# Optimization experiments

Measured on AMD Instinct MI355X. Metric: run time of the kernel, lower is better.

## Reference

```python
import jax, jax.numpy as jnp
import numpy as np

B, S, D, H = 4, 1024, 1024, 16
DK = D // H


def _linear_params(key, scale):
    kw, kb = jax.random.split(key)
    W = jax.random.normal(kw, (D, D), dtype=jnp.float32) * scale
    b = jax.random.normal(kb, (D,), dtype=jnp.float32) * 0.01
    return W, b


def setup_inputs() -> dict:
    key = jax.random.key(0)
    ks = jax.random.split(key, 12)
    scale = 1.0 / np.sqrt(D)
    inp = {
        "query": jax.random.normal(ks[0], (B, S, D), dtype=jnp.float32),
        "key": jax.random.normal(ks[1], (B, S, D), dtype=jnp.float32),
        "value": jax.random.normal(ks[2], (B, S, D), dtype=jnp.float32),
        "time_k": jax.random.normal(ks[3], (B, S, D), dtype=jnp.float32),
        "time_v": jax.random.normal(ks[4], (B, S, D), dtype=jnp.float32),
        "mask": jnp.zeros((B, 1, S, S), dtype=jnp.float32),
    }
    names = ["Wq", "bq", "Wk", "bk", "Wv", "bv", "Wtk", "btk", "Wtv", "btv", "Wm", "bm"]
    for i in range(6):
        W, b = _linear_params(ks[5 + i], scale)
        inp[names[2 * i]] = W
        inp[names[2 * i + 1]] = b
    return inp


def _split_heads(x):
    # [B,S,D] -> [B,H,S,DK]
    b, s, _ = x.shape
    return x.reshape(b, s, H, DK).transpose(0, 2, 1, 3)


def reference(query, key, value, time_k, time_v, mask,
              Wq, bq, Wk, bk, Wv, bv, Wtk, btk, Wtv, btv, Wm, bm):
    q = _split_heads(query @ Wq + bq)
    k = _split_heads(key @ Wk + bk)
    v = _split_heads(value @ Wv + bv)
    t_k = _split_heads(time_k @ Wtk + btk)
    t_v = _split_heads(time_v @ Wtv + btv)

    # scores[b,h,i,j] = q_i . k_j + t_k_i . q_j  (note second term uses q on the key axis)
    scores = jnp.einsum("bhid,bhjd->bhij", q, k) + jnp.einsum("bhid,bhjd->bhij", t_k, q)
    # module divides by sqrt(d_model) (query.size(-1)), not sqrt(d_k)
    scores = scores / jnp.sqrt(jnp.float32(D)) + mask
    probs = jax.nn.softmax(scores, axis=-1)

    # dropout is identity (p=0 / eval); squeeze(-2) is a no-op for S>1
    context = jnp.einsum("bhij,bhjd->bhid", probs, v) + jnp.einsum("bhij,bhjd->bhid", probs, t_v)
    x = context.transpose(0, 2, 1, 3).reshape(query.shape[0], -1, D)
    return x @ Wm + bm
```

## Files before the change

kernel.cpp:

```cpp
#include <hip/hip_runtime.h>
#include <hip/hip_bf16.h>
#include <cstdint>
#include <cstddef>

typedef __bf16 bf16;
typedef bf16 bf16x8 __attribute__((ext_vector_type(8)));
typedef bf16 bf16x4 __attribute__((ext_vector_type(4)));
typedef float f32x4 __attribute__((ext_vector_type(4)));
typedef unsigned int u32;

#define DEV static __device__ __forceinline__

DEV f32x4 mfma16(bf16x8 a, bf16x8 b, f32x4 c) {
    return __builtin_amdgcn_mfma_f32_16x16x32_bf16(a, b, c, 0, 0, 0);
}

DEV f32x4 shflx4(f32x4 v, int m) {
    f32x4 r;
    for (int i = 0; i < 4; ++i) r[i] = __shfl_xor(v[i], m, 64);
    return r;
}

DEV bf16x8 cvt8(const float* p) {
    float4 f0 = *(const float4*)p;
    float4 f1 = *(const float4*)(p + 4);
    bf16x8 v;
    v[0] = (bf16)f0.x; v[1] = (bf16)f0.y; v[2] = (bf16)f0.z; v[3] = (bf16)f0.w;
    v[4] = (bf16)f1.x; v[5] = (bf16)f1.y; v[6] = (bf16)f1.z; v[7] = (bf16)f1.w;
    return v;
}

DEV void glo(const bf16* g, bf16* l) {
    __builtin_amdgcn_global_load_lds(
        (const __attribute__((address_space(1))) u32*)g,
        (__attribute__((address_space(3))) u32*)l,
        16, 0, 0);
}

struct PrepArgs {
    const float* w[10];
    const float* act[5];
    bf16* wt;
    bf16* maskt;
    bf16* actbf[5];
};

__global__ __launch_bounds__(256) void prep_kernel(PrepArgs p)
{
    const int z = blockIdx.z;
    const int t = threadIdx.x;
    if (z < 10) {
        __shared__ bf16 tile[64][72];
        const float* src = p.w[z];
        bf16* out = (z < 6) ? (p.wt + (size_t)z * 1024 * 1024)
                            : (p.maskt + (size_t)(z - 6) * 1024 * 1024);
        const int r = t >> 3, c8 = (t & 7) * 8;
        const int row0 = blockIdx.y * 64, col0 = blockIdx.x * 64;
        *(bf16x8*)&tile[r][c8]      = cvt8(&src[(size_t)(row0 + r) * 1024 + col0 + c8]);
        *(bf16x8*)&tile[r + 32][c8] = cvt8(&src[(size_t)(row0 + r + 32) * 1024 + col0 + c8]);
        __syncthreads();
        for (int half = 0; half < 2; ++half) {
            int rr = r + half * 32;
            bf16x8 v;
            for (int j = 0; j < 8; ++j) v[j] = tile[c8 + j][rr];
            *(bf16x8*)&out[(size_t)(col0 + rr) * 1024 + row0 + c8] = v;
        }
    } else {
        const float* src = p.act[z - 10];
        bf16* dst = p.actbf[z - 10];
        const size_t chunk = (size_t)(blockIdx.y * 16 + blockIdx.x) * 16384;
        for (int c = 0; c < 8; ++c) {
            const size_t off = chunk + (size_t)c * 2048 + (size_t)t * 8;
            *(bf16x8*)&dst[off] = cvt8(&src[off]);
        }
    }
}

__global__ __launch_bounds__(256) void vsum_kernel(bf16* __restrict__ a,
                                                   const bf16* __restrict__ b)
{
    const size_t off = ((size_t)blockIdx.x * 256 + threadIdx.x) * 16;
    for (int c = 0; c < 2; ++c) {
        bf16x8 x = *(const bf16x8*)&a[off + c * 8];
        bf16x8 y = *(const bf16x8*)&b[off + c * 8];
        bf16x8 s;
        for (int e = 0; e < 8; ++e) s[e] = (bf16)((float)x[e] + (float)y[e]);
        *(bf16x8*)&a[off + c * 8] = s;
    }
}

struct ProjArgs {
    const void* A[5];
    const void* A2[5];
    const bf16* W[5];
    const bf16* W2[5];
    const float* bias[5];
    const float* bias2[5];
    bf16* out[5];
    int vst[5];
};

template<bool AF32>
__global__ __launch_bounds__(256) void proj_gemm(ProjArgs pa)
{
    const int z = blockIdx.z;
    const void* A   = pa.A[z];
    const void* A2p = pa.A2[z];
    const bf16* W   = pa.W[z];
    const bf16* W2  = pa.W2[z];
    const int m0 = blockIdx.y * 128, n0 = blockIdx.x * 128;
    __shared__ bf16 As[128 * 64];
    __shared__ bf16 Bs[128 * 64];
    const int t = threadIdx.x, lane = t & 63, w = t >> 6;
    const int ln = lane & 15, qd = lane >> 4;
    const int wm0 = (w >> 1) * 64, wn0 = (w & 1) * 64;
    const int srow = t >> 1, shalf = (t & 1) * 32;
    const int sub0 = w * 4;
    const int r8 = lane >> 3, c8 = (lane & 7) * 8;
    f32x4 acc[4][4];
    for (int i = 0; i < 4; ++i)
        for (int j = 0; j < 4; ++j)
            acc[i][j] = (f32x4){0.f, 0.f, 0.f, 0.f};
    const int npair = A2p ? 2 : 1;
    for (int pair = 0; pair < npair; ++pair) {
        const void* Ap = pair ? A2p : A;
        const bf16* Wp = pair ? W2 : W;
        for (int ks = 0; ks < 16; ++ks) {
            const int bk = ks * 64;
            __syncthreads();
            for (int i = 0; i < 4; ++i) {
                const int row = (sub0 + i) * 8 + r8;
                glo(&Wp[(size_t)(n0 + row) * 1024 + bk + c8], &Bs[(sub0 + i) * 512]);
            }
            if (AF32) {
                const float* src = &((const float*)Ap)[(size_t)(m0 + srow) * 1024 + bk + shalf];
                bf16* dst = &As[srow * 64 + shalf];
                *(bf16x8*)(dst)      = cvt8(src);
                *(bf16x8*)(dst + 8)  = cvt8(src + 8);
                *(bf16x8*)(dst + 16) = cvt8(src + 16);
                *(bf16x8*)(dst + 24) = cvt8(src + 24);
            } else {
                const bf16* Ab = (const bf16*)Ap;
                for (int i = 0; i < 4; ++i) {
                    const int row = (sub0 + i) * 8 + r8;
                    glo(&Ab[(size_t)(m0 + row) * 1024 + bk + c8], &As[(sub0 + i) * 512]);
                }
            }
            __syncthreads();
            for (int kc = 0; kc < 2; ++kc) {
                bf16x8 af[4], bfr[4];
                for (int mi = 0; mi < 4; ++mi)
                    af[mi] = *(const bf16x8*)&As[(wm0 + mi * 16 + ln) * 64 + kc * 32 + qd * 8];
                for (int ni = 0; ni < 4; ++ni)
                    bfr[ni] = *(const bf16x8*)&Bs[(wn0 + ni * 16 + ln) * 64 + kc * 32 + qd * 8];
                for (int mi = 0; mi < 4; ++mi)
                    for (int ni = 0; ni < 4; ++ni)
                        acc[mi][ni] = mfma16(af[mi], bfr[ni], acc[mi][ni]);
            }
        }
    }
    const float* bias  = pa.bias[z];
    const float* bias2 = pa.bias2[z];
    bf16* out = pa.out[z];
    const int vst = pa.vst[z];
    for (int ni = 0; ni < 4; ++ni) {
        const int n = n0 + wn0 + ni * 16 + ln;
        const float bv = bias[n] + (bias2 ? bias2[n] : 0.0f);
        for (int mi = 0; mi < 4; ++mi) {
            const int mbase = m0 + wm0 + mi * 16 + qd * 4;
            f32x4 v = acc[mi][ni];
            if (vst) {
                const int b = mbase >> 10, s = mbase & 1023;
                bf16x4 pk;
                for (int r = 0; r < 4; ++r) pk[r] = (bf16)(v[r] + bv);
                *(bf16x4*)&out[((size_t)(b * 1024 + n)) * 1024 + s] = pk;
            } else {
                for (int r = 0; r < 4; ++r)
                    out[(size_t)(mbase + r) * 1024 + n] = (bf16)(v[r] + bv);
            }
        }
    }
}

__global__ __launch_bounds__(256, 4) void attn5_kernel(
    const bf16* __restrict__ Qb, const bf16* __restrict__ Kb, const bf16* __restrict__ TKb,
    const bf16* __restrict__ VsT, const bf16* __restrict__ maskT,
    bf16* __restrict__ ctx)
{
    const int h = blockIdx.x, it = blockIdx.y, b = blockIdx.z;
    const int i0 = it * 64;
    __shared__ bf16 Ks[64 * 64];
    __shared__ bf16 QJs[64 * 64];
    __shared__ bf16 Vs[64 * 64];
    __shared__ bf16 Ps[64][68];
    const int t = threadIdx.x, lane = t & 63, w = t >> 6;
    const int ln = lane & 15, qd = lane >> 4;
    const size_t baseQ = ((size_t)b * 1024) * 1024 + (size_t)h * 64;
    const size_t MMc = (size_t)1024 * 1024;

    bf16x8 qf[2], tkf[2];
    {
        const size_t row = (size_t)(i0 + w * 16 + ln);
        for (int kc = 0; kc < 2; ++kc) {
            qf[kc]  = *(const bf16x8*)&Qb [baseQ + row * 1024 + kc * 32 + qd * 8];
            tkf[kc] = *(const bf16x8*)&TKb[baseQ + row * 1024 + kc * 32 + qd * 8];
        }
    }

    f32x4 O[4];
    f32x4 psum = (f32x4){0.f, 0.f, 0.f, 0.f};
    for (int dc = 0; dc < 4; ++dc) O[dc] = (f32x4){0.f, 0.f, 0.f, 0.f};

    const float c1 = 0.045084439f;
    const float c2 = 1.442695041f;

    for (int jt = 0; jt < 16; ++jt) {
        const int j0 = jt * 64;
        __syncthreads();
        {
            const int rr = lane >> 3, cb = (lane & 7) * 8;
            for (int i = 0; i < 6; ++i) {
                const int u = w * 6 + i;
                if (u < 8) {
                    glo(&Kb[baseQ + (size_t)(j0 + u * 8 + rr) * 1024 + cb], &Ks[u * 512]);
                } else if (u < 16) {
                    const int s = u - 8;
                    glo(&Qb[baseQ + (size_t)(j0 + s * 8 + rr) * 1024 + cb], &QJs[s * 512]);
                } else {
                    const int s = u - 16;
                    glo(&VsT[((size_t)b * 1024 + h * 64 + s * 8 + rr) * 1024 + j0 + cb],
                        &Vs[s * 512]);
                }
            }
        }
        bf16x4 mv[4];
        {
            const int ibase = i0 + w * 16 + qd * 4;
            for (int jc = 0; jc < 4; ++jc)
                mv[jc] = *(const bf16x4*)&maskT[(size_t)b * MMc +
                          (size_t)(j0 + jc * 16 + ln) * 1024 + ibase];
        }
        __syncthreads();

        f32x4 sc[4];
        for (int jc = 0; jc < 4; ++jc) {
            bf16x8 kf[2], qjf[2];
            for (int kc = 0; kc < 2; ++kc) {
                kf[kc]  = *(const bf16x8*)&Ks [(jc * 16 + ln) * 64 + kc * 32 + qd * 8];
                qjf[kc] = *(const bf16x8*)&QJs[(jc * 16 + ln) * 64 + kc * 32 + qd * 8];
            }
            f32x4 a = (f32x4){0.f, 0.f, 0.f, 0.f};
            a = mfma16(qf[0], kf[0], a);
            a = mfma16(qf[1], kf[1], a);
            a = mfma16(tkf[0], qjf[0], a);
            a = mfma16(tkf[1], qjf[1], a);
            sc[jc] = a;
        }
        const int ibl = w * 16 + qd * 4;
        for (int jc = 0; jc < 4; ++jc) {
            const int jl = jc * 16 + ln;
            for (int r = 0; r < 4; ++r) {
                const float p = exp2f(fmaf(sc[jc][r], c1, (float)mv[jc][r] * c2));
                psum[r] += p;
                Ps[ibl + r][jl] = (bf16)p;
            }
        }
        for (int kc = 0; kc < 2; ++kc) {
            bf16x4 lo = *(const bf16x4*)&Ps[w * 16 + ln][kc * 32 + qd * 8];
            bf16x4 hi = *(const bf16x4*)&Ps[w * 16 + ln][kc * 32 + qd * 8 + 4];
            bf16x8 pa;
            for (int e = 0; e < 4; ++e) { pa[e] = lo[e]; pa[4 + e] = hi[e]; }
            for (int dc = 0; dc < 4; ++dc) {
                bf16x8 vf = *(const bf16x8*)&Vs[(dc * 16 + ln) * 64 + kc * 32 + qd * 8];
                O[dc] = mfma16(pa, vf, O[dc]);
            }
        }
    }

    for (int m = 1; m <= 8; m <<= 1) psum += shflx4(psum, m);
    f32x4 rl;
    for (int r = 0; r < 4; ++r) rl[r] = 1.0f / psum[r];
    const int ibase = i0 + w * 16 + qd * 4;
    for (int dc = 0; dc < 4; ++dc) {
        const int d = h * 64 + dc * 16 + ln;
        f32x4 v = O[dc] * rl;
        for (int r = 0; r < 4; ++r)
            ctx[((size_t)b * 1024 + ibase + r) * 1024 + d] = (bf16)v[r];
    }
}

__global__ __launch_bounds__(256) void out_gemm(
    const bf16* __restrict__ A, const bf16* __restrict__ W,
    const float* __restrict__ bias, float* __restrict__ out)
{
    const int n0 = blockIdx.x * 128, m0 = blockIdx.y * 64;
    __shared__ bf16 As[64 * 64];
    __shared__ bf16 Bs[128 * 64];
    const int t = threadIdx.x, lane = t & 63, w = t >> 6;
    const int ln = lane & 15, qd = lane >> 4;
    const int wn0 = w * 32;
    const int rr = lane >> 3, cb = (lane & 7) * 8;
    f32x4 acc[4][2];
    for (int i = 0; i < 4; ++i)
        for (int j = 0; j < 2; ++j)
            acc[i][j] = (f32x4){0.f, 0.f, 0.f, 0.f};
    for (int ks = 0; ks < 16; ++ks) {
        const int bk = ks * 64;
        __syncthreads();
        for (int i = 0; i < 6; ++i) {
            const int u = w * 6 + i;
            if (u < 8) {
                const int r8 = u * 8 + rr;
                glo(&A[(size_t)(m0 + r8) * 1024 + bk + cb], &As[u * 512]);
            } else {
                const int sub = u - 8, r8 = sub * 8 + rr;
                glo(&W[(size_t)(n0 + r8) * 1024 + bk + cb], &Bs[sub * 512]);
            }
        }
        __syncthreads();
        for (int kc = 0; kc < 2; ++kc) {
            bf16x8 af[4], bfr[2];
            for (int mi = 0; mi < 4; ++mi)
                af[mi] = *(const bf16x8*)&As[(mi * 16 + ln) * 64 + kc * 32 + qd * 8];
            for (int ni = 0; ni < 2; ++ni)
                bfr[ni] = *(const bf16x8*)&Bs[(wn0 + ni * 16 + ln) * 64 + kc * 32 + qd * 8];
            for (int mi = 0; mi < 4; ++mi)
                for (int ni = 0; ni < 2; ++ni)
                    acc[mi][ni] = mfma16(af[mi], bfr[ni], acc[mi][ni]);
        }
    }
    for (int ni = 0; ni < 2; ++ni) {
        const int n = n0 + wn0 + ni * 16 + ln;
        const float bv = bias[n];
        for (int mi = 0; mi < 4; ++mi) {
            const int mbase = m0 + mi * 16 + qd * 4;
            f32x4 v = acc[mi][ni];
            for (int r = 0; r < 4; ++r)
                out[(size_t)(mbase + r) * 1024 + n] = v[r] + bv;
        }
    }
}

extern "C" void kernel_launch(void* const* d_in, const int* in_sizes, int n_in,
                              void* d_out, int out_size, void* d_ws, size_t ws_size,
                              hipStream_t stream)
{
    (void)in_sizes; (void)n_in; (void)out_size;
    const float* query  = (const float*)d_in[0];
    const float* key    = (const float*)d_in[1];
    const float* value  = (const float*)d_in[2];
    const float* time_k = (const float*)d_in[3];
    const float* time_v = (const float*)d_in[4];
    const float* mask   = (const float*)d_in[5];
    const float* Wq  = (const float*)d_in[6];  const float* bq  = (const float*)d_in[7];
    const float* Wk  = (const float*)d_in[8];  const float* bk  = (const float*)d_in[9];
    const float* Wv  = (const float*)d_in[10]; const float* bv  = (const float*)d_in[11];
    const float* Wtk = (const float*)d_in[12]; const float* btk = (const float*)d_in[13];
    const float* Wtv = (const float*)d_in[14]; const float* btv = (const float*)d_in[15];
    const float* Wm  = (const float*)d_in[16]; const float* bm  = (const float*)d_in[17];

    bf16* ws = (bf16*)d_ws;
    const size_t MM = (size_t)1024 * 1024;
    bf16* WT = ws;
    bf16* maskT = (bf16*)d_out;

    PrepArgs pp;
    pp.w[0] = Wq; pp.w[1] = Wk; pp.w[2] = Wv; pp.w[3] = Wtk; pp.w[4] = Wtv; pp.w[5] = Wm;
    for (int b = 0; b < 4; ++b) pp.w[6 + b] = mask + (size_t)b * MM;
    pp.wt = WT;
    pp.maskt = maskT;

    const bool big = ws_size >= (size_t)(46 * MM * sizeof(bf16));

    if (big) {
        bf16* qbf  = ws + 6 * MM;
        bf16* kbf  = ws + 10 * MM;
        bf16* vbf  = ws + 14 * MM;
        bf16* tkbf = ws + 18 * MM;
        bf16* tvbf = ws + 22 * MM;
        bf16* Qb   = ws + 26 * MM;
        bf16* Kb   = ws + 30 * MM;
        bf16* TKb  = ws + 34 * MM;
        bf16* VsTa = ws + 38 * MM;
        bf16* VsTb = ws + 42 * MM;
        bf16* ctx  = ws + 6 * MM;
        pp.act[0] = query; pp.act[1] = key; pp.act[2] = value;
        pp.act[3] = time_k; pp.act[4] = time_v;
        pp.actbf[0] = qbf; pp.actbf[1] = kbf; pp.actbf[2] = vbf;
        pp.actbf[3] = tkbf; pp.actbf[4] = tvbf;
        prep_kernel<<<dim3(16, 16, 15), 256, 0, stream>>>(pp);

        ProjArgs pa;
        for (int i = 0; i < 5; ++i) { pa.A2[i] = nullptr; pa.W2[i] = nullptr; pa.bias2[i] = nullptr; }
        pa.A[0] = qbf;  pa.W[0] = WT + 0 * MM; pa.bias[0] = bq;  pa.out[0] = Qb;   pa.vst[0] = 0;
        pa.A[1] = kbf;  pa.W[1] = WT + 1 * MM; pa.bias[1] = bk;  pa.out[1] = Kb;   pa.vst[1] = 0;
        pa.A[2] = tkbf; pa.W[2] = WT + 3 * MM; pa.bias[2] = btk; pa.out[2] = TKb;  pa.vst[2] = 0;
        pa.A[3] = vbf;  pa.W[3] = WT + 2 * MM; pa.bias[3] = bv;  pa.out[3] = VsTa; pa.vst[3] = 1;
        pa.A[4] = tvbf; pa.W[4] = WT + 4 * MM; pa.bias[4] = btv; pa.out[4] = VsTb; pa.vst[4] = 1;
        proj_gemm<false><<<dim3(8, 32, 5), 256, 0, stream>>>(pa);

        vsum_kernel<<<dim3(1024), 256, 0, stream>>>(VsTa, VsTb);
        attn5_kernel<<<dim3(16, 16, 4), 256, 0, stream>>>(
            Qb, Kb, TKb, VsTa, maskT, ctx);
        out_gemm<<<dim3(8, 64), 256, 0, stream>>>(ctx, WT + 5 * MM, bm, (float*)d_out);
    } else {
        bf16* Qb  = ws + 6 * MM;
        bf16* Kb  = ws + 10 * MM;
        bf16* TKb = ws + 14 * MM;
        bf16* VsT = ws + 18 * MM;
        bf16* ctx = ws + 22 * MM;
        for (int i = 0; i < 5; ++i) { pp.act[i] = nullptr; pp.actbf[i] = nullptr; }
        prep_kernel<<<dim3(16, 16, 10), 256, 0, stream>>>(pp);

        ProjArgs pa;
        for (int i = 0; i < 5; ++i) { pa.A2[i] = nullptr; pa.W2[i] = nullptr; pa.bias2[i] = nullptr; }
        pa.A[0] = value;  pa.A2[0] = time_v; pa.W[0] = WT + 2 * MM; pa.W2[0] = WT + 4 * MM;
        pa.bias[0] = bv;  pa.bias2[0] = btv; pa.out[0] = VsT; pa.vst[0] = 1;
        pa.A[1] = query;  pa.W[1] = WT + 0 * MM; pa.bias[1] = bq;  pa.out[1] = Qb;  pa.vst[1] = 0;
        pa.A[2] = key;    pa.W[2] = WT + 1 * MM; pa.bias[2] = bk;  pa.out[2] = Kb;  pa.vst[2] = 0;
        pa.A[3] = time_k; pa.W[3] = WT + 3 * MM; pa.bias[3] = btk; pa.out[3] = TKb; pa.vst[3] = 0;
        proj_gemm<true><<<dim3(8, 32, 4), 256, 0, stream>>>(pa);

        attn5_kernel<<<dim3(16, 16, 4), 256, 0, stream>>>(
            Qb, Kb, TKb, VsT, maskT, ctx);
        out_gemm<<<dim3(8, 64), 256, 0, stream>>>(ctx, WT + 5 * MM, bm, (float*)d_out);
    }
}
```

Baseline: 342.9 us.

## Fuse fp32-to-bf16 activation conversion into projection GEMM and pad A tile

```diff
diff --git a/kernel.cpp b/kernel.cpp
--- a/kernel.cpp
+++ b/kernel.cpp
@@ -39,40 +39,28 @@
 
 struct PrepArgs {
     const float* w[10];
-    const float* act[5];
     bf16* wt;
     bf16* maskt;
-    bf16* actbf[5];
 };
 
 __global__ __launch_bounds__(256) void prep_kernel(PrepArgs p)
 {
     const int z = blockIdx.z;
     const int t = threadIdx.x;
-    if (z < 10) {
-        __shared__ bf16 tile[64][72];
-        const float* src = p.w[z];
-        bf16* out = (z < 6) ? (p.wt + (size_t)z * 1024 * 1024)
-                            : (p.maskt + (size_t)(z - 6) * 1024 * 1024);
-        const int r = t >> 3, c8 = (t & 7) * 8;
-        const int row0 = blockIdx.y * 64, col0 = blockIdx.x * 64;
-        *(bf16x8*)&tile[r][c8]      = cvt8(&src[(size_t)(row0 + r) * 1024 + col0 + c8]);
-        *(bf16x8*)&tile[r + 32][c8] = cvt8(&src[(size_t)(row0 + r + 32) * 1024 + col0 + c8]);
-        __syncthreads();
-        for (int half = 0; half < 2; ++half) {
-            int rr = r + half * 32;
-            bf16x8 v;
-            for (int j = 0; j < 8; ++j) v[j] = tile[c8 + j][rr];
-            *(bf16x8*)&out[(size_t)(col0 + rr) * 1024 + row0 + c8] = v;
-        }
-    } else {
-        const float* src = p.act[z - 10];
-        bf16* dst = p.actbf[z - 10];
-        const size_t chunk = (size_t)(blockIdx.y * 16 + blockIdx.x) * 16384;
-        for (int c = 0; c < 8; ++c) {
-            const size_t off = chunk + (size_t)c * 2048 + (size_t)t * 8;
-            *(bf16x8*)&dst[off] = cvt8(&src[off]);
-        }
+    __shared__ bf16 tile[64][72];
+    const float* src = p.w[z];
+    bf16* out = (z < 6) ? (p.wt + (size_t)z * 1024 * 1024)
+                        : (p.maskt + (size_t)(z - 6) * 1024 * 1024);
+    const int r = t >> 3, c8 = (t & 7) * 8;
+    const int row0 = blockIdx.y * 64, col0 = blockIdx.x * 64;
+    *(bf16x8*)&tile[r][c8]      = cvt8(&src[(size_t)(row0 + r) * 1024 + col0 + c8]);
+    *(bf16x8*)&tile[r + 32][c8] = cvt8(&src[(size_t)(row0 + r + 32) * 1024 + col0 + c8]);
+    __syncthreads();
+    for (int half = 0; half < 2; ++half) {
+        int rr = r + half * 32;
+        bf16x8 v;
+        for (int j = 0; j < 8; ++j) v[j] = tile[c8 + j][rr];
+        *(bf16x8*)&out[(size_t)(col0 + rr) * 1024 + row0 + c8] = v;
     }
 }
 
@@ -90,26 +78,20 @@
 }
 
 struct ProjArgs {
-    const void* A[5];
-    const void* A2[5];
-    const bf16* W[5];
-    const bf16* W2[5];
+    const float* A[5];
+    const bf16*  W[5];
     const float* bias[5];
-    const float* bias2[5];
     bf16* out[5];
     int vst[5];
 };
 
-template<bool AF32>
 __global__ __launch_bounds__(256) void proj_gemm(ProjArgs pa)
 {
     const int z = blockIdx.z;
-    const void* A   = pa.A[z];
-    const void* A2p = pa.A2[z];
-    const bf16* W   = pa.W[z];
-    const bf16* W2  = pa.W2[z];
+    const float* A = pa.A[z];
+    const bf16*  W = pa.W[z];
     const int m0 = blockIdx.y * 128, n0 = blockIdx.x * 128;
-    __shared__ bf16 As[128 * 64];
+    __shared__ bf16 As[128 * 72];
     __shared__ bf16 Bs[128 * 64];
     const int t = threadIdx.x, lane = t & 63, w = t >> 6;
     const int ln = lane & 15, qd = lane >> 4;
@@ -121,51 +103,39 @@
     for (int i = 0; i < 4; ++i)
         for (int j = 0; j < 4; ++j)
             acc[i][j] = (f32x4){0.f, 0.f, 0.f, 0.f};
-    const int npair = A2p ? 2 : 1;
-    for (int pair = 0; pair < npair; ++pair) {
-        const void* Ap = pair ? A2p : A;
-        const bf16* Wp = pair ? W2 : W;
-        for (int ks = 0; ks < 16; ++ks) {
-            const int bk = ks * 64;
-            __syncthreads();
-            for (int i = 0; i < 4; ++i) {
-                const int row = (sub0 + i) * 8 + r8;
-                glo(&Wp[(size_t)(n0 + row) * 1024 + bk + c8], &Bs[(sub0 + i) * 512]);
-            }
-            if (AF32) {
-                const float* src = &((const float*)Ap)[(size_t)(m0 + srow) * 1024 + bk + shalf];
-                bf16* dst = &As[srow * 64 + shalf];
-                *(bf16x8*)(dst)      = cvt8(src);
-                *(bf16x8*)(dst + 8)  = cvt8(src + 8);
-                *(bf16x8*)(dst + 16) = cvt8(src + 16);
-                *(bf16x8*)(dst + 24) = cvt8(src + 24);
-            } else {
-                const bf16* Ab = (const bf16*)Ap;
-                for (int i = 0; i < 4; ++i) {
-                    const int row = (sub0 + i) * 8 + r8;
-                    glo(&Ab[(size_t)(m0 + row) * 1024 + bk + c8], &As[(sub0 + i) * 512]);
-                }
-            }
-            __syncthreads();
-            for (int kc = 0; kc < 2; ++kc) {
-                bf16x8 af[4], bfr[4];
-                for (int mi = 0; mi < 4; ++mi)
-                    af[mi] = *(const bf16x8*)&As[(wm0 + mi * 16 + ln) * 64 + kc * 32 + qd * 8];
+    for (int ks = 0; ks < 16; ++ks) {
+        const int bk = ks * 64;
+        __syncthreads();
+        for (int i = 0; i < 4; ++i) {
+            const int row = (sub0 + i) * 8 + r8;
+            glo(&W[(size_t)(n0 + row) * 1024 + bk + c8], &Bs[(sub0 + i) * 512]);
+        }
+        {
+            const float* src = &A[(size_t)(m0 + srow) * 1024 + bk + shalf];
+            bf16* dst = &As[srow * 72 + shalf];
+            *(bf16x8*)(dst)      = cvt8(src);
+            *(bf16x8*)(dst + 8)  = cvt8(src + 8);
+            *(bf16x8*)(dst + 16) = cvt8(src + 16);
+            *(bf16x8*)(dst + 24) = cvt8(src + 24);
+        }
+        __syncthreads();
+        for (int kc = 0; kc < 2; ++kc) {
+            bf16x8 af[4], bfr[4];
+            for (int mi = 0; mi < 4; ++mi)
+                af[mi] = *(const bf16x8*)&As[(wm0 + mi * 16 + ln) * 72 + kc * 32 + qd * 8];
+            for (int ni = 0; ni < 4; ++ni)
+                bfr[ni] = *(const bf16x8*)&Bs[(wn0 + ni * 16 + ln) * 64 + kc * 32 + qd * 8];
+            for (int mi = 0; mi < 4; ++mi)
                 for (int ni = 0; ni < 4; ++ni)
-                    bfr[ni] = *(const bf16x8*)&Bs[(wn0 + ni * 16 + ln) * 64 + kc * 32 + qd * 8];
-                for (int mi = 0; mi < 4; ++mi)
-                    for (int ni = 0; ni < 4; ++ni)
-                        acc[mi][ni] = mfma16(af[mi], bfr[ni], acc[mi][ni]);
-            }
-        }
-    }
-    const float* bias  = pa.bias[z];
-    const float* bias2 = pa.bias2[z];
+                    acc[mi][ni] = mfma16(af[mi], bfr[ni], acc[mi][ni]);
+        }
+    }
+    const float* bias = pa.bias[z];
     bf16* out = pa.out[z];
     const int vst = pa.vst[z];
     for (int ni = 0; ni < 4; ++ni) {
         const int n = n0 + wn0 + ni * 16 + ln;
-        const float bv = bias[n] + (bias2 ? bias2[n] : 0.0f);
+        const float bv = bias[n];
         for (int mi = 0; mi < 4; ++mi) {
             const int mbase = m0 + wm0 + mi * 16 + qd * 4;
             f32x4 v = acc[mi][ni];
@@ -345,7 +315,7 @@
                               void* d_out, int out_size, void* d_ws, size_t ws_size,
                               hipStream_t stream)
 {
-    (void)in_sizes; (void)n_in; (void)out_size;
+    (void)in_sizes; (void)n_in; (void)out_size; (void)ws_size;
     const float* query  = (const float*)d_in[0];
     const float* key    = (const float*)d_in[1];
     const float* value  = (const float*)d_in[2];
@@ -361,7 +331,13 @@
 
     bf16* ws = (bf16*)d_ws;
     const size_t MM = (size_t)1024 * 1024;
-    bf16* WT = ws;
+    bf16* WT    = ws;
+    bf16* Qb    = ws + 6 * MM;
+    bf16* Kb    = ws + 10 * MM;
+    bf16* TKb   = ws + 14 * MM;
+    bf16* VsTa  = ws + 18 * MM;
+    bf16* VsTb  = ws + 22 * MM;
+    bf16* ctx   = ws + 26 * MM;
     bf16* maskT = (bf16*)d_out;
 
     PrepArgs pp;
@@ -369,60 +345,17 @@
     for (int b = 0; b < 4; ++b) pp.w[6 + b] = mask + (size_t)b * MM;
     pp.wt = WT;
     pp.maskt = maskT;
-
-    const bool big = ws_size >= (size_t)(46 * MM * sizeof(bf16));
-
-    if (big) {
-        bf16* qbf  = ws + 6 * MM;
-        bf16* kbf  = ws + 10 * MM;
-        bf16* vbf  = ws + 14 * MM;
-        bf16* tkbf = ws + 18 * MM;
-        bf16* tvbf = ws + 22 * MM;
-        bf16* Qb   = ws + 26 * MM;
-        bf16* Kb   = ws + 30 * MM;
-        bf16* TKb  = ws + 34 * MM;
-        bf16* VsTa = ws + 38 * MM;
-        bf16* VsTb = ws + 42 * MM;
-        bf16* ctx  = ws + 6 * MM;
-        pp.act[0] = query; pp.act[1] = key; pp.act[2] = value;
-        pp.act[3] = time_k; pp.act[4] = time_v;
-        pp.actbf[0] = qbf; pp.actbf[1] = kbf; pp.actbf[2] = vbf;
-        pp.actbf[3] = tkbf; pp.actbf[4] = tvbf;
-        prep_kernel<<<dim3(16, 16, 15), 256, 0, stream>>>(pp);
-
-        ProjArgs pa;
-        for (int i = 0; i < 5; ++i) { pa.A2[i] = nullptr; pa.W2[i] = nullptr; pa.bias2[i] = nullptr; }
-        pa.A[0] = qbf;  pa.W[0] = WT + 0 * MM; pa.bias[0] = bq;  pa.out[0] = Qb;   pa.vst[0] = 0;
-        pa.A[1] = kbf;  pa.W[1] = WT + 1 * MM; pa.bias[1] = bk;  pa.out[1] = Kb;   pa.vst[1] = 0;
-        pa.A[2] = tkbf; pa.W[2] = WT + 3 * MM; pa.bias[2] = btk; pa.out[2] = TKb;  pa.vst[2] = 0;
-        pa.A[3] = vbf;  pa.W[3] = WT + 2 * MM; pa.bias[3] = bv;  pa.out[3] = VsTa; pa.vst[3] = 1;
-        pa.A[4] = tvbf; pa.W[4] = WT + 4 * MM; pa.bias[4] = btv; pa.out[4] = VsTb; pa.vst[4] = 1;
-        proj_gemm<false><<<dim3(8, 32, 5), 256, 0, stream>>>(pa);
-
-        vsum_kernel<<<dim3(1024), 256, 0, stream>>>(VsTa, VsTb);
-        attn5_kernel<<<dim3(16, 16, 4), 256, 0, stream>>>(
-            Qb, Kb, TKb, VsTa, maskT, ctx);
-        out_gemm<<<dim3(8, 64), 256, 0, stream>>>(ctx, WT + 5 * MM, bm, (float*)d_out);
-    } else {
-        bf16* Qb  = ws + 6 * MM;
-        bf16* Kb  = ws + 10 * MM;
-        bf16* TKb = ws + 14 * MM;
-        bf16* VsT = ws + 18 * MM;
-        bf16* ctx = ws + 22 * MM;
-        for (int i = 0; i < 5; ++i) { pp.act[i] = nullptr; pp.actbf[i] = nullptr; }
-        prep_kernel<<<dim3(16, 16, 10), 256, 0, stream>>>(pp);
-
-        ProjArgs pa;
-        for (int i = 0; i < 5; ++i) { pa.A2[i] = nullptr; pa.W2[i] = nullptr; pa.bias2[i] = nullptr; }
-        pa.A[0] = value;  pa.A2[0] = time_v; pa.W[0] = WT + 2 * MM; pa.W2[0] = WT + 4 * MM;
-        pa.bias[0] = bv;  pa.bias2[0] = btv; pa.out[0] = VsT; pa.vst[0] = 1;
-        pa.A[1] = query;  pa.W[1] = WT + 0 * MM; pa.bias[1] = bq;  pa.out[1] = Qb;  pa.vst[1] = 0;
-        pa.A[2] = key;    pa.W[2] = WT + 1 * MM; pa.bias[2] = bk;  pa.out[2] = Kb;  pa.vst[2] = 0;
-        pa.A[3] = time_k; pa.W[3] = WT + 3 * MM; pa.bias[3] = btk; pa.out[3] = TKb; pa.vst[3] = 0;
-        proj_gemm<true><<<dim3(8, 32, 4), 256, 0, stream>>>(pa);
-
-        attn5_kernel<<<dim3(16, 16, 4), 256, 0, stream>>>(
-            Qb, Kb, TKb, VsT, maskT, ctx);
-        out_gemm<<<dim3(8, 64), 256, 0, stream>>>(ctx, WT + 5 * MM, bm, (float*)d_out);
-    }
-}
+    prep_kernel<<<dim3(16, 16, 10), 256, 0, stream>>>(pp);
+
+    ProjArgs pa;
+    pa.A[0] = query;  pa.W[0] = WT + 0 * MM; pa.bias[0] = bq;  pa.out[0] = Qb;   pa.vst[0] = 0;
+    pa.A[1] = key;    pa.W[1] = WT + 1 * MM; pa.bias[1] = bk;  pa.out[1] = Kb;   pa.vst[1] = 0;
+    pa.A[2] = time_k; pa.W[2] = WT + 3 * MM; pa.bias[2] = btk; pa.out[2] = TKb;  pa.vst[2] = 0;
+    pa.A[3] = value;  pa.W[3] = WT + 2 * MM; pa.bias[3] = bv;  pa.out[3] = VsTa; pa.vst[3] = 1;
+    pa.A[4] = time_v; pa.W[4] = WT + 4 * MM; pa.bias[4] = btv; pa.out[4] = VsTb; pa.vst[4] = 1;
+    proj_gemm<<<dim3(8, 32, 5), 256, 0, stream>>>(pa);
+
+    vsum_kernel<<<dim3(1024), 256, 0, stream>>>(VsTa, VsTb);
+    attn5_kernel<<<dim3(16, 16, 4), 256, 0, stream>>>(Qb, Kb, TKb, VsTa, maskT, ctx);
+    out_gemm<<<dim3(8, 64), 256, 0, stream>>>(ctx, WT + 5 * MM, bm, (float*)d_out);
+}
```

Measured after the change: 373.9 us. +9.0%, slower.
